# Performance work log

Measured on AMD Instinct MI355X. Metric: run time of the kernel, lower is better.

The kernel has to match this reference:

```python
import jax, jax.numpy as jnp
import numpy as np
from jax import lax

FEAT_STRIDE = 16
SCALES = np.array([8, 16, 32], dtype=np.float64)
RATIOS = np.array([0.5, 1, 2], dtype=np.float64)
PRE_NMS_TOP_N = 6000
POST_NMS_TOP_N = 1000
NMS_THRESH = 0.7

# ---- anchor generation (numpy, static constants) ----

def _whctrs(a):
    w = a[2] - a[0] + 1.0
    h = a[3] - a[1] + 1.0
    return w, h, a[0] + 0.5 * (w - 1.0), a[1] + 0.5 * (h - 1.0)

def _mkanchors(ws, hs, xc, yc):
    return np.stack([xc - 0.5 * (ws - 1.0), yc - 0.5 * (hs - 1.0),
                     xc + 0.5 * (ws - 1.0), yc + 0.5 * (hs - 1.0)], axis=1)

def _ratio_enum(anchor, ratios):
    w, h, xc, yc = _whctrs(anchor)
    size = w * h
    ws = np.round(np.sqrt(size / ratios))
    hs = np.round(ws * ratios)
    return _mkanchors(ws, hs, xc, yc)

def _scale_enum(anchor, scales):
    w, h, xc, yc = _whctrs(anchor)
    return _mkanchors(w * scales, h * scales, xc, yc)

def generate_anchors(base_size=16):
    base = np.array([1, 1, base_size, base_size], dtype=np.float64) - 1.0
    ra = _ratio_enum(base, RATIOS)
    return np.vstack([_scale_enum(ra[i], SCALES) for i in range(ra.shape[0])]).astype(np.float32)


def setup_inputs() -> dict:
    key = jax.random.key(0)
    k1, k2 = jax.random.split(key)
    H, W, A = 76, 128, 9
    scores = jax.random.uniform(k1, (1, 2 * A, H, W), dtype=jnp.float32)
    bbox_delta = jax.random.normal(k2, (1, 4 * A, H, W), dtype=jnp.float32) * 0.1
    im_info = jnp.array([H * FEAT_STRIDE, W * FEAT_STRIDE, 1.0], dtype=jnp.float32)  # [h, w, scale]
    return {"scores": scores, "bbox_delta": bbox_delta, "im_info": im_info}


def reference(scores, bbox_delta, im_info):
    anchors = generate_anchors()            # [A, 4]
    A = anchors.shape[0]
    H, W = scores.shape[2], scores.shape[3]

    # grid of shifted anchors: [K*A, 4], anchor index varies fastest (matches permute layout)
    sx = np.arange(W) * FEAT_STRIDE
    sy = np.arange(H) * FEAT_STRIDE
    sx, sy = np.meshgrid(sx, sy)
    shifts = np.stack([sx.ravel(), sy.ravel(), sx.ravel(), sy.ravel()], axis=1).astype(np.float32)  # [K,4]
    all_anchors = jnp.asarray((anchors[None, :, :] + shifts[:, None, :]).reshape(-1, 4))  # [K*A,4]

    # foreground scores, NHWC flatten -> [K*A]
    fg = jnp.transpose(scores[0, A:], (1, 2, 0)).reshape(-1)
    # deltas, NHWC flatten -> [K*A, 4]
    deltas = jnp.transpose(bbox_delta[0], (1, 2, 0)).reshape(-1, 4)

    aw = all_anchors[:, 2] - all_anchors[:, 0] + 1.0
    ah = all_anchors[:, 3] - all_anchors[:, 1] + 1.0
    acx = all_anchors[:, 0] + 0.5 * aw
    acy = all_anchors[:, 1] + 0.5 * ah
    pcx = deltas[:, 0] * aw + acx
    pcy = deltas[:, 1] * ah + acy
    pw = jnp.exp(deltas[:, 2]) * aw
    ph = jnp.exp(deltas[:, 3]) * ah
    boxes = jnp.stack([pcx - 0.5 * pw, pcy - 0.5 * ph, pcx + 0.5 * pw, pcy + 0.5 * ph], axis=1)

    # clip_boxes to image
    xmax = im_info[1] - 1.0
    ymax = im_info[0] - 1.0
    boxes = jnp.stack([jnp.clip(boxes[:, 0], 0.0, xmax), jnp.clip(boxes[:, 1], 0.0, ymax),
                       jnp.clip(boxes[:, 2], 0.0, xmax), jnp.clip(boxes[:, 3], 0.0, ymax)], axis=1)

    # pre-NMS top-N by fg score
    top_scores, top_idx = lax.top_k(fg, PRE_NMS_TOP_N)
    props = boxes[top_idx]                  # [N, 4], sorted by score desc

    # pairwise IoU (+1 convention)
    x1, y1, x2, y2 = props[:, 0], props[:, 1], props[:, 2], props[:, 3]
    areas = (x2 - x1 + 1.0) * (y2 - y1 + 1.0)
    iw = jnp.clip(jnp.minimum(x2[:, None], x2[None, :]) - jnp.maximum(x1[:, None], x1[None, :]) + 1.0, 0.0)
    ih = jnp.clip(jnp.minimum(y2[:, None], y2[None, :]) - jnp.maximum(y1[:, None], y1[None, :]) + 1.0, 0.0)
    inter = iw * ih
    iou = inter / (areas[:, None] + areas[None, :] - inter)  # [N, N]

    # sequential greedy NMS over score-sorted boxes
    N = PRE_NMS_TOP_N
    later = jnp.arange(N)
    def body(i, keep):
        sup = (iou[i] > NMS_THRESH) & keep[i] & (later > i)
        return keep & ~sup
    keep = lax.fori_loop(0, N, body, jnp.ones((N,), dtype=bool))

    masked = jnp.where(keep, top_scores, -jnp.inf)
    _, sel = lax.top_k(masked, POST_NMS_TOP_N)
    return props[sel]                       # [POST_NMS_TOP_N, 4]
```

## Files before the change

kernel.cpp:

```cpp
#include <hip/hip_runtime.h>
#include <cstdint>

#define HH 76
#define WW 128
#define AA 9
#define HWH (HH * WW)
#define KK (HWH * AA)
#define NSEL 6000
#define NCH 94
#define NPAD (NCH * 64)
#define NOUT 1000
#define NMS_T 0.7
#define NTRI (NCH * (NCH + 1) / 2)
#define MASK_BLOCKS 1117
#define SELCAP 16384
#define BINCAP 2048
#define HIST_BLOCKS 22
#define NBIN 16384

#define LBAR() asm volatile("s_waitcnt lgkmcnt(0)\n\ts_barrier" ::: "memory")

#define WS_HIST 0
#define WS_BINB 65536
#define WS_NACT 65540
#define WS_DONE1 65544
#define WS_ZERO_BYTES 65552
#define WS_ACTIVE 65552
#define WS_BINBASE 98320
#define WS_SELKEYS 163856
#define WS_BOXES 294928
#define WS_MASK 391184

__device__ __constant__ float c_ax1[9] = {-84.f, -176.f, -360.f, -56.f, -120.f, -248.f, -36.f, -80.f, -168.f};
__device__ __constant__ float c_ay1[9] = {-40.f, -88.f, -184.f, -56.f, -120.f, -248.f, -80.f, -168.f, -344.f};
__device__ __constant__ float c_ax2[9] = {99.f, 191.f, 375.f, 71.f, 135.f, 263.f, 51.f, 95.f, 183.f};
__device__ __constant__ float c_ay2[9] = {55.f, 103.f, 199.f, 71.f, 135.f, 263.f, 95.f, 183.f, 359.f};

__device__ __forceinline__ unsigned score_key(float s) {
    unsigned u = __float_as_uint(s);
    return (u & 0x80000000u) ? ~u : (u | 0x80000000u);
}

__device__ __forceinline__ int key_bin(unsigned key) {
    int bi = (int)(key >> 16) - 0x8000;
    return bi < 0 ? 0 : (bi > NBIN - 1 ? NBIN - 1 : bi);
}

__device__ __forceinline__ unsigned long long chunk_scan_fix(unsigned long long col,
                                                             unsigned long long alive_in) {
    unsigned long long kept = alive_in;
    while (true) {
        unsigned long long sup = __ballot((int)((col & kept) != 0ull));
        unsigned long long kept2 = alive_in & ~sup;
        if (kept2 == kept) return kept;
        kept = kept2;
    }
}

__global__ __launch_bounds__(1024) void k_zero(unsigned* __restrict__ ws32) {
    int i = blockIdx.x * 1024 + threadIdx.x;
    if (i < (int)(WS_ZERO_BYTES / 4)) ws32[i] = 0;
}

__global__ __launch_bounds__(1024) void k_histfind(const float* __restrict__ scores,
                                                   unsigned* __restrict__ histG,
                                                   unsigned* __restrict__ binB,
                                                   unsigned* __restrict__ binBase,
                                                   unsigned* __restrict__ activeList,
                                                   unsigned* __restrict__ nact,
                                                   unsigned* __restrict__ done) {
    __shared__ unsigned hloc[NBIN];
    int t = threadIdx.x;
#pragma unroll
    for (int k = 0; k < NBIN / 1024; ++k) hloc[t + k * 1024] = 0;
    __syncthreads();
    int gid = blockIdx.x * 1024 + t;
    if (gid < KK / 4) {
        float4 v = ((const float4*)(scores + AA * HWH))[gid];
        atomicAdd(&hloc[key_bin(score_key(v.x))], 1u);
        atomicAdd(&hloc[key_bin(score_key(v.y))], 1u);
        atomicAdd(&hloc[key_bin(score_key(v.z))], 1u);
        atomicAdd(&hloc[key_bin(score_key(v.w))], 1u);
    }
    __syncthreads();
#pragma unroll
    for (int k = 0; k < NBIN / 1024; ++k) {
        unsigned c = hloc[t + k * 1024];
        if (c) atomicAdd(&histG[t + k * 1024], c);
    }
    __threadfence();
    __shared__ unsigned lastS;
    if (t == 0) lastS = (atomicAdd(done, 1u) == (unsigned)gridDim.x - 1u) ? 1u : 0u;
    __syncthreads();
    if (!lastS) return;
    __threadfence();

    __shared__ unsigned seg[1024];
    __shared__ unsigned Bsh;
    unsigned local[16];
    unsigned ssum = 0;
#pragma unroll
    for (int k = 0; k < 16; ++k) { local[k] = histG[t * 16 + k]; ssum += local[k]; }
    seg[t] = ssum;
    __syncthreads();
    for (int off = 1; off < 1024; off <<= 1) {
        unsigned v = seg[t];
        unsigned add = (t + off < 1024) ? seg[t + off] : 0u;
        __syncthreads();
        seg[t] = v + add;
        __syncthreads();
    }
    unsigned above = (t + 1 < 1024) ? seg[t + 1] : 0u;
    if (above < NSEL && above + ssum >= NSEL) {
        unsigned acc = above;
#pragma unroll
        for (int b = 15; b >= 0; --b) {
            acc += local[b];
            if (acc >= NSEL) { Bsh = (unsigned)(t * 16 + b); *binB = Bsh; break; }
        }
    }
    __syncthreads();
    unsigned B = Bsh;
    if ((unsigned)(t * 16 + 15) >= B) {
        unsigned acc2 = above;
        for (int k = 15; k >= 0; --k) {
            unsigned bin = (unsigned)(t * 16 + k);
            if (bin < B) break;
            if (local[k] > 0) {
                binBase[bin] = acc2;
                unsigned tick = atomicAdd(nact, 1u);
                if (tick < 8192) activeList[tick] = bin;
            }
            acc2 += local[k];
        }
    }
}

__global__ __launch_bounds__(1024) void k_gather(const float* __restrict__ scores,
                                                 const unsigned* __restrict__ binB,
                                                 unsigned* __restrict__ binBase,
                                                 unsigned long long* __restrict__ selKeys) {
    int j4 = blockIdx.x * 1024 + threadIdx.x;
    if (j4 >= KK / 4) return;
    float4 v = ((const float4*)(scores + AA * HWH))[j4];
    unsigned B = *binB;
    float sv[4] = {v.x, v.y, v.z, v.w};
#pragma unroll
    for (int k = 0; k < 4; ++k) {
        int j = j4 * 4 + k;
        unsigned key = score_key(sv[k]);
        unsigned bin = (unsigned)key_bin(key);
        if (bin >= B) {
            int a = j / HWH;
            int hw = j - a * HWH;
            unsigned i = (unsigned)(hw * AA + a);
            unsigned pos = atomicAdd(&binBase[bin], 1u);
            if (pos < SELCAP)
                selKeys[pos] = ((unsigned long long)key << 32) | (unsigned)(~i);
        }
    }
}

__global__ __launch_bounds__(256) void k_binsort(const unsigned* __restrict__ histG,
                                                 const unsigned* __restrict__ binBase,
                                                 const unsigned* __restrict__ activeList,
                                                 const unsigned* __restrict__ nact,
                                                 unsigned long long* __restrict__ selKeys,
                                                 const float* __restrict__ bbox,
                                                 const float* __restrict__ im_info,
                                                 float4* __restrict__ boxes) {
    __shared__ unsigned long long sk[BINCAP];
    int t = threadIdx.x;
    unsigned na = *nact;
    if (na > 8192) na = 8192;
    double xmax = (double)im_info[1] - 1.0, ymax = (double)im_info[0] - 1.0;
    for (unsigned aIdx = blockIdx.x; aIdx < na; aIdx += gridDim.x) {
        unsigned bin = activeList[aIdx];
        unsigned ntot = histG[bin];
        unsigned base = binBase[bin] - ntot;
        unsigned n = ntot > BINCAP ? BINCAP : ntot;
        unsigned m = 64; while (m < n) m <<= 1;
        for (unsigned p = t; p < m; p += 256) sk[p] = (p < n) ? selKeys[base + p] : 0ull;
        __syncthreads();
        for (unsigned size = 2; size <= m; size <<= 1) {
            for (unsigned stride = size >> 1; stride > 0; stride >>= 1) {
                for (unsigned p = (unsigned)t; p < m / 2; p += 256) {
                    unsigned i = 2u * p - (p & (stride - 1u));
                    unsigned j = i + stride;
                    bool up = (i & size) != 0;
                    unsigned long long a = sk[i], b = sk[j];
                    bool doswap = up ? (a > b) : (a < b);
                    if (doswap) { sk[i] = b; sk[j] = a; }
                }
                __syncthreads();
            }
        }
        for (unsigned r = t; r < n; r += 256) {
            unsigned g = base + r;
            if (g >= NSEL) continue;
            unsigned i = ~(unsigned)(sk[r] & 0xFFFFFFFFull);
            int a = (int)(i % AA);
            int hw = (int)(i / AA);
            int h = hw >> 7, w = hw & 127;
            double sx = 16.0 * w, sy = 16.0 * h;
            double ax1 = (double)c_ax1[a] + sx, ay1 = (double)c_ay1[a] + sy;
            double ax2 = (double)c_ax2[a] + sx, ay2 = (double)c_ay2[a] + sy;
            double aw = ax2 - ax1 + 1.0, ah = ay2 - ay1 + 1.0;
            double acx = ax1 + 0.5 * aw, acy = ay1 + 0.5 * ah;
            int bse = h * WW + w;
            double d0 = (double)bbox[(4 * a + 0) * HWH + bse];
            double d1 = (double)bbox[(4 * a + 1) * HWH + bse];
            double d2 = (double)bbox[(4 * a + 2) * HWH + bse];
            double d3 = (double)bbox[(4 * a + 3) * HWH + bse];
            double pcx = d0 * aw + acx, pcy = d1 * ah + acy;
            double pw = exp(d2) * aw, ph = exp(d3) * ah;
            double x1 = fmin(fmax(pcx - 0.5 * pw, 0.0), xmax);
            double y1 = fmin(fmax(pcy - 0.5 * ph, 0.0), ymax);
            double x2 = fmin(fmax(pcx + 0.5 * pw, 0.0), xmax);
            double y2 = fmin(fmax(pcy + 0.5 * ph, 0.0), ymax);
            boxes[g] = make_float4((float)x1, (float)y1, (float)x2, (float)y2);
        }
        __syncthreads();
    }
}

__global__ __launch_bounds__(256) void k_mask(const float4* __restrict__ boxes,
                                              unsigned long long* __restrict__ supT) {
    __shared__ float4 cb[4][64];
    int wave = threadIdx.x >> 6, lane = threadIdx.x & 63;
    for (int L = blockIdx.x * 4 + wave; L < NTRI; L += MASK_BLOCKS * 4) {
        int rc = 0, rem = L;
        while (rem >= NCH - rc) { rem -= NCH - rc; rc++; }
        int cc = rc + rem;
        cb[wave][lane] = boxes[cc * 64 + lane];
        int gi = rc * 64 + lane;
        unsigned long long bits = 0ull;
        if (gi < NSEL) {
            float4 rb = boxes[gi];
            double rx1 = rb.x, ry1 = rb.y, rx2 = rb.z, ry2 = rb.w;
            double rarea = (rx2 - rx1 + 1.0) * (ry2 - ry1 + 1.0);
            for (int j = 0; j < 64; ++j) {
                int gj = cc * 64 + j;
                float4 c = cb[wave][j];
                double iw = fmin(rx2, (double)c.z) - fmax(rx1, (double)c.x) + 1.0;
                double ih = fmin(ry2, (double)c.w) - fmax(ry1, (double)c.y) + 1.0;
                if (gj > gi && gj < NSEL && iw > 0.0 && ih > 0.0) {
                    double inter = iw * ih;
                    double carea = ((double)c.z - (double)c.x + 1.0) * ((double)c.w - (double)c.y + 1.0);
                    double uni = rarea + carea - inter;
                    if (inter > NMS_T * uni) bits |= (1ull << j);
                }
            }
        }
        unsigned long long myword = 0ull;
        for (int j = 0; j < 64; ++j) {
            unsigned long long bal = __ballot((int)((bits >> j) & 1ull));
            if (lane == j) myword = bal;
        }
        supT[(size_t)rc * NPAD + cc * 64 + lane] = myword;
    }
}

__global__ __launch_bounds__(512, 1) void k_nms(const unsigned long long* __restrict__ supT,
                                                const float4* __restrict__ boxes,
                                                float4* __restrict__ out) {
    __shared__ unsigned long long colLds[NCH][64];
    __shared__ unsigned long long removed[NCH];
    __shared__ unsigned long long aliveArr[NCH];
    __shared__ int cstop;
    __shared__ unsigned scanBuf[8];
    int t = threadIdx.x;
    int wave = t >> 6, lane = t & 63;

    for (int c = wave; c < NCH; c += 8)
        colLds[c][lane] = supT[(size_t)c * NPAD + c * 64 + lane];
    for (int i = t; i < NCH; i += 512) removed[i] = (i == NCH - 1) ? 0xFFFF000000000000ull : 0ull;
    if (t == 0) cstop = -1;
    __syncthreads();
    if (wave == 0) __builtin_amdgcn_s_setprio(1);

    unsigned long long wAA = 0, wAB = 0;
    unsigned long long mA[8], mB[8];
#pragma unroll
    for (int q = 0; q < 8; ++q) { mA[q] = 0; mB[q] = 0; }
    if (wave == 0) wAA = supT[(size_t)0 * NPAD + 1 * 64 + lane];
    unsigned keptTot = 0;

    for (int c = 0; c < NCH; c += 2) {
        if (wave == 0) {
            if (c + 2 < NCH) wAB = supT[(size_t)(c + 1) * NPAD + (c + 2) * 64 + lane];
            unsigned long long alive_in = ~removed[c];
            unsigned long long alive = chunk_scan_fix(colLds[c][lane], alive_in);
            keptTot += (unsigned)__popcll(alive);
            if (lane == 0) {
                removed[c] = ~alive;
                aliveArr[c] = alive;
                if (keptTot >= NOUT) cstop = c;
            }
            if (c + 1 < NCH) {
                unsigned long long ball = __ballot((int)((wAA & alive) != 0ull));
                if (lane == 0 && ball) atomicOr(&removed[c + 1], ball);
            }
        } else {
            if (c + 2 < NCH) {
#pragma unroll
                for (int q = 0; q < 8; ++q) {
                    int cp = (wave - 1) + 7 * q;
                    mB[q] = (cp < c + 1) ? supT[(size_t)cp * NPAD + (c + 2) * 64 + lane] : 0ull;
                }
            }
            if (c + 1 < NCH) {
                unsigned long long acc = 0ull;
#pragma unroll
                for (int q = 0; q < 8; ++q) {
                    int cp = (wave - 1) + 7 * q;
                    if (cp < c) acc |= __ballot((int)((mA[q] & aliveArr[cp]) != 0ull));
                }
                for (int cp = (wave - 1) + 56; cp < c; cp += 7) {
                    unsigned long long wv = supT[(size_t)cp * NPAD + (c + 1) * 64 + lane];
                    acc |= __ballot((int)((wv & aliveArr[cp]) != 0ull));
                }
                if (lane == 0 && acc) atomicOr(&removed[c + 1], acc);
            }
        }
        LBAR();
        if (cstop >= 0) break;
        if (c + 1 >= NCH) break;

        if (wave == 0) {
            if (c + 3 < NCH) wAA = supT[(size_t)(c + 2) * NPAD + (c + 3) * 64 + lane];
            unsigned long long alive_in = ~removed[c + 1];
            unsigned long long alive = chunk_scan_fix(colLds[c + 1][lane], alive_in);
            keptTot += (unsigned)__popcll(alive);
            if (lane == 0) {
                removed[c + 1] = ~alive;
                aliveArr[c + 1] = alive;
                if (keptTot >= NOUT) cstop = c + 1;
            }
            if (c + 2 < NCH) {
                unsigned long long ball = __ballot((int)((wAB & alive) != 0ull));
                if (lane == 0 && ball) atomicOr(&removed[c + 2], ball);
            }
        } else {
            if (c + 3 < NCH) {
#pragma unroll
                for (int q = 0; q < 8; ++q) {
                    int cp = (wave - 1) + 7 * q;
                    mA[q] = (cp < c + 2) ? supT[(size_t)cp * NPAD + (c + 3) * 64 + lane] : 0ull;
                }
            }
            if (c + 2 < NCH) {
                unsigned long long acc = 0ull;
#pragma unroll
                for (int q = 0; q < 8; ++q) {
                    int cp = (wave - 1) + 7 * q;
                    if (cp < c + 1) acc |= __ballot((int)((mB[q] & aliveArr[cp]) != 0ull));
                }
                for (int cp = (wave - 1) + 56; cp < c + 1; cp += 7) {
                    unsigned long long wv = supT[(size_t)cp * NPAD + (c + 2) * 64 + lane];
                    acc |= __ballot((int)((wv & aliveArr[cp]) != 0ull));
                }
                if (lane == 0 && acc) atomicOr(&removed[c + 2], acc);
            }
        }
        LBAR();
        if (cstop >= 0) break;
    }
    if (wave == 0) __builtin_amdgcn_s_setprio(0);
    __syncthreads();

    int base = t * 12;
    unsigned cnt = 0, keepbits = 0;
    for (int q = 0; q < 12; ++q) {
        int i = base + q;
        if (i < NSEL) {
            bool kp = !((removed[i >> 6] >> (i & 63)) & 1ull);
            if (kp) { cnt++; keepbits |= (1u << q); }
        }
    }
    unsigned v = cnt;
#pragma unroll
    for (int off = 1; off < 64; off <<= 1) {
        unsigned u = (unsigned)__shfl_up((int)v, off, 64);
        if (lane >= off) v += u;
    }
    if (lane == 63) scanBuf[wave] = v;
    __syncthreads();
    unsigned waveOff = 0, NK = 0;
#pragma unroll
    for (int ww = 0; ww < 8; ++ww) {
        unsigned wv = scanBuf[ww];
        if (ww < wave) waveOff += wv;
        NK += wv;
    }
    unsigned incl = waveOff + v;
    unsigned kpos = incl - cnt;
    for (int q = 0; q < 12; ++q) {
        int i = base + q;
        if (i < NSEL) {
            bool kp = (keepbits >> q) & 1u;
            unsigned pos = kp ? kpos : (NK + (unsigned)i - kpos);
            if (kp) kpos++;
            if (pos < NOUT) out[pos] = boxes[i];
        }
    }
}

extern "C" void kernel_launch(void* const* d_in, const int* in_sizes, int n_in,
                              void* d_out, int out_size, void* d_ws, size_t ws_size,
                              hipStream_t stream) {
    const float* scores = (const float*)d_in[0];
    const float* bbox = (const float*)d_in[1];
    const float* im_info = (const float*)d_in[2];
    char* ws = (char*)d_ws;

    unsigned* histG = (unsigned*)(ws + WS_HIST);
    unsigned* binB = (unsigned*)(ws + WS_BINB);
    unsigned* nact = (unsigned*)(ws + WS_NACT);
    unsigned* done1 = (unsigned*)(ws + WS_DONE1);
    unsigned* activeList = (unsigned*)(ws + WS_ACTIVE);
    unsigned* binBase = (unsigned*)(ws + WS_BINBASE);
    unsigned long long* selKeys = (unsigned long long*)(ws + WS_SELKEYS);
    float4* boxes = (float4*)(ws + WS_BOXES);
    unsigned long long* supT = (unsigned long long*)(ws + WS_MASK);
    float4* out = (float4*)d_out;

    k_zero<<<17, 1024, 0, stream>>>((unsigned*)ws);
    k_histfind<<<HIST_BLOCKS, 1024, 0, stream>>>(scores, histG, binB, binBase, activeList, nact, done1);
    k_gather<<<HIST_BLOCKS, 1024, 0, stream>>>(scores, binB, binBase, selKeys);
    k_binsort<<<64, 256, 0, stream>>>(histG, binBase, activeList, nact, selKeys, bbox, im_info, boxes);
    k_mask<<<MASK_BLOCKS, 256, 0, stream>>>(boxes, supT);
    k_nms<<<1, 512, 0, stream>>>(supT, boxes, out);
}
```

Baseline: 116.0 us.

## Fuse histogram and gather kernels using in-kernel grid barrier with spin flag

Merges the histogram/threshold kernel and the gather kernel into one launch. The last-arriving block computes the prefix scan and bin bases, then publishes a release flag. The other blocks spin on that flag and reuse their already-loaded score registers to scatter the selected keys. This removes one kernel launch and the second read of the scores array. It relies on all 22 blocks being co-resident for the spin-wait to avoid deadlock, and it reuses the shared histogram buffer as scan scratch.

```diff
diff --git a/kernel.cpp b/kernel.cpp
--- a/kernel.cpp
+++ b/kernel.cpp
@@ -15,7 +15,7 @@
 #define MASK_BLOCKS 1117
 #define SELCAP 16384
 #define BINCAP 2048
-#define HIST_BLOCKS 22
+#define FRONT_BLOCKS 22
 #define NBIN 16384
 
 #define LBAR() asm volatile("s_waitcnt lgkmcnt(0)\n\ts_barrier" ::: "memory")
@@ -23,7 +23,8 @@
 #define WS_HIST 0
 #define WS_BINB 65536
 #define WS_NACT 65540
-#define WS_DONE1 65544
+#define WS_ARRIVE 65544
+#define WS_FLAG 65548
 #define WS_ZERO_BYTES 65552
 #define WS_ACTIVE 65552
 #define WS_BINBASE 98320
@@ -62,21 +63,25 @@
     if (i < (int)(WS_ZERO_BYTES / 4)) ws32[i] = 0;
 }
 
-__global__ __launch_bounds__(1024) void k_histfind(const float* __restrict__ scores,
-                                                   unsigned* __restrict__ histG,
-                                                   unsigned* __restrict__ binB,
-                                                   unsigned* __restrict__ binBase,
-                                                   unsigned* __restrict__ activeList,
-                                                   unsigned* __restrict__ nact,
-                                                   unsigned* __restrict__ done) {
+__global__ __launch_bounds__(1024) void k_front(const float* __restrict__ scores,
+                                                unsigned* __restrict__ histG,
+                                                unsigned* __restrict__ binB,
+                                                unsigned* __restrict__ binBase,
+                                                unsigned* __restrict__ activeList,
+                                                unsigned* __restrict__ nact,
+                                                unsigned* __restrict__ arrive,
+                                                unsigned* __restrict__ flag,
+                                                unsigned long long* __restrict__ selKeys) {
     __shared__ unsigned hloc[NBIN];
     int t = threadIdx.x;
 #pragma unroll
     for (int k = 0; k < NBIN / 1024; ++k) hloc[t + k * 1024] = 0;
     __syncthreads();
     int gid = blockIdx.x * 1024 + t;
-    if (gid < KK / 4) {
-        float4 v = ((const float4*)(scores + AA * HWH))[gid];
+    bool haveV = gid < KK / 4;
+    float4 v = make_float4(0.f, 0.f, 0.f, 0.f);
+    if (haveV) {
+        v = ((const float4*)(scores + AA * HWH))[gid];
         atomicAdd(&hloc[key_bin(score_key(v.x))], 1u);
         atomicAdd(&hloc[key_bin(score_key(v.y))], 1u);
         atomicAdd(&hloc[key_bin(score_key(v.z))], 1u);
@@ -90,73 +95,79 @@
     }
     __threadfence();
     __shared__ unsigned lastS;
-    if (t == 0) lastS = (atomicAdd(done, 1u) == (unsigned)gridDim.x - 1u) ? 1u : 0u;
-    __syncthreads();
-    if (!lastS) return;
-    __threadfence();
-
-    __shared__ unsigned seg[1024];
-    __shared__ unsigned Bsh;
-    unsigned local[16];
-    unsigned ssum = 0;
-#pragma unroll
-    for (int k = 0; k < 16; ++k) { local[k] = histG[t * 16 + k]; ssum += local[k]; }
-    seg[t] = ssum;
-    __syncthreads();
-    for (int off = 1; off < 1024; off <<= 1) {
-        unsigned v = seg[t];
-        unsigned add = (t + off < 1024) ? seg[t + off] : 0u;
-        __syncthreads();
-        seg[t] = v + add;
-        __syncthreads();
-    }
-    unsigned above = (t + 1 < 1024) ? seg[t + 1] : 0u;
-    if (above < NSEL && above + ssum >= NSEL) {
-        unsigned acc = above;
-#pragma unroll
-        for (int b = 15; b >= 0; --b) {
-            acc += local[b];
-            if (acc >= NSEL) { Bsh = (unsigned)(t * 16 + b); *binB = Bsh; break; }
-        }
-    }
-    __syncthreads();
-    unsigned B = Bsh;
-    if ((unsigned)(t * 16 + 15) >= B) {
-        unsigned acc2 = above;
-        for (int k = 15; k >= 0; --k) {
-            unsigned bin = (unsigned)(t * 16 + k);
-            if (bin < B) break;
-            if (local[k] > 0) {
-                binBase[bin] = acc2;
-                unsigned tick = atomicAdd(nact, 1u);
-                if (tick < 8192) activeList[tick] = bin;
-            }
-            acc2 += local[k];
-        }
-    }
-}
-
-__global__ __launch_bounds__(1024) void k_gather(const float* __restrict__ scores,
-                                                 const unsigned* __restrict__ binB,
-                                                 unsigned* __restrict__ binBase,
-                                                 unsigned long long* __restrict__ selKeys) {
-    int j4 = blockIdx.x * 1024 + threadIdx.x;
-    if (j4 >= KK / 4) return;
-    float4 v = ((const float4*)(scores + AA * HWH))[j4];
-    unsigned B = *binB;
-    float sv[4] = {v.x, v.y, v.z, v.w};
-#pragma unroll
-    for (int k = 0; k < 4; ++k) {
-        int j = j4 * 4 + k;
-        unsigned key = score_key(sv[k]);
-        unsigned bin = (unsigned)key_bin(key);
-        if (bin >= B) {
-            int a = j / HWH;
-            int hw = j - a * HWH;
-            unsigned i = (unsigned)(hw * AA + a);
-            unsigned pos = atomicAdd(&binBase[bin], 1u);
-            if (pos < SELCAP)
-                selKeys[pos] = ((unsigned long long)key << 32) | (unsigned)(~i);
+    if (t == 0) lastS = (atomicAdd(arrive, 1u) == (unsigned)FRONT_BLOCKS - 1u) ? 1u : 0u;
+    __syncthreads();
+
+    if (lastS) {
+        __threadfence();
+        unsigned* seg = hloc;
+        __shared__ unsigned Bsh;
+        unsigned local[16];
+        unsigned ssum = 0;
+        __syncthreads();
+#pragma unroll
+        for (int k = 0; k < 16; ++k) { local[k] = histG[t * 16 + k]; ssum += local[k]; }
+        seg[t] = ssum;
+        __syncthreads();
+        for (int off = 1; off < 1024; off <<= 1) {
+            unsigned vv = seg[t];
+            unsigned add = (t + off < 1024) ? seg[t + off] : 0u;
+            __syncthreads();
+            seg[t] = vv + add;
+            __syncthreads();
+        }
+        unsigned above = (t + 1 < 1024) ? seg[t + 1] : 0u;
+        if (above < NSEL && above + ssum >= NSEL) {
+            unsigned acc = above;
+#pragma unroll
+            for (int b = 15; b >= 0; --b) {
+                acc += local[b];
+                if (acc >= NSEL) { Bsh = (unsigned)(t * 16 + b); *binB = Bsh; break; }
+            }
+        }
+        __syncthreads();
+        unsigned B = Bsh;
+        if ((unsigned)(t * 16 + 15) >= B) {
+            unsigned acc2 = above;
+            for (int k = 15; k >= 0; --k) {
+                unsigned bin = (unsigned)(t * 16 + k);
+                if (bin < B) break;
+                if (local[k] > 0) {
+                    binBase[bin] = acc2;
+                    unsigned tick = atomicAdd(nact, 1u);
+                    if (tick < 8192) activeList[tick] = bin;
+                }
+                acc2 += local[k];
+            }
+        }
+        __syncthreads();
+        __threadfence();
+        if (t == 0) __hip_atomic_store(flag, 1u, __ATOMIC_RELEASE, __HIP_MEMORY_SCOPE_AGENT);
+    } else {
+        if (t == 0) {
+            while (!__hip_atomic_load(flag, __ATOMIC_ACQUIRE, __HIP_MEMORY_SCOPE_AGENT))
+                __builtin_amdgcn_s_sleep(1);
+        }
+        __syncthreads();
+        __threadfence();
+    }
+
+    if (haveV) {
+        unsigned B = *binB;
+        float sv[4] = {v.x, v.y, v.z, v.w};
+#pragma unroll
+        for (int k = 0; k < 4; ++k) {
+            int j = gid * 4 + k;
+            unsigned key = score_key(sv[k]);
+            unsigned bin = (unsigned)key_bin(key);
+            if (bin >= B) {
+                int a = j / HWH;
+                int hw = j - a * HWH;
+                unsigned i = (unsigned)(hw * AA + a);
+                unsigned pos = atomicAdd(&binBase[bin], 1u);
+                if (pos < SELCAP)
+                    selKeys[pos] = ((unsigned long long)key << 32) | (unsigned)(~i);
+            }
         }
     }
 }
@@ -417,7 +428,8 @@
     unsigned* histG = (unsigned*)(ws + WS_HIST);
     unsigned* binB = (unsigned*)(ws + WS_BINB);
     unsigned* nact = (unsigned*)(ws + WS_NACT);
-    unsigned* done1 = (unsigned*)(ws + WS_DONE1);
+    unsigned* arrive = (unsigned*)(ws + WS_ARRIVE);
+    unsigned* flag = (unsigned*)(ws + WS_FLAG);
     unsigned* activeList = (unsigned*)(ws + WS_ACTIVE);
     unsigned* binBase = (unsigned*)(ws + WS_BINBASE);
     unsigned long long* selKeys = (unsigned long long*)(ws + WS_SELKEYS);
@@ -426,8 +438,8 @@
     float4* out = (float4*)d_out;
 
     k_zero<<<17, 1024, 0, stream>>>((unsigned*)ws);
-    k_histfind<<<HIST_BLOCKS, 1024, 0, stream>>>(scores, histG, binB, binBase, activeList, nact, done1);
-    k_gather<<<HIST_BLOCKS, 1024, 0, stream>>>(scores, binB, binBase, selKeys);
+    k_front<<<FRONT_BLOCKS, 1024, 0, stream>>>(scores, histG, binB, binBase, activeList,
+                                               nact, arrive, flag, selKeys);
     k_binsort<<<64, 256, 0, stream>>>(histG, binBase, activeList, nact, selKeys, bbox, im_info, boxes);
     k_mask<<<MASK_BLOCKS, 256, 0, stream>>>(boxes, supT);
     k_nms<<<1, 512, 0, stream>>>(supT, boxes, out);
```

After: 125.2 us. 7.9% more time.
